# Kernel optimization log

Measured on AMD Instinct MI355X. Metric: run time of the kernel, lower is better.

The kernel has to match this reference:

```python
import jax, jax.numpy as jnp
import numpy as np

B, T, HID = 4, 2048, 1024
NH = 16
HS = HID // NH  # 64


def setup_inputs() -> dict:
    key = jax.random.key(0)
    ks = jax.random.split(key, 9)
    s = 1.0 / np.sqrt(HID)
    return {
        "x": jax.random.normal(ks[0], (B, T, HID), dtype=jnp.float32),
        "Wq": jax.random.uniform(ks[1], (HID, HID), jnp.float32, -s, s),
        "bq": jax.random.uniform(ks[2], (HID,), jnp.float32, -s, s),
        "Wk": jax.random.uniform(ks[3], (HID, HID), jnp.float32, -s, s),
        "bk": jax.random.uniform(ks[4], (HID,), jnp.float32, -s, s),
        "Wv": jax.random.uniform(ks[5], (HID, HS), jnp.float32, -s, s),
        "bv": jax.random.uniform(ks[6], (HS,), jnp.float32, -s, s),
        "Wo": jax.random.uniform(ks[7], (HS, HID), jnp.float32, -1.0 / np.sqrt(HS), 1.0 / np.sqrt(HS)),
        "bo": jax.random.uniform(ks[8], (HID,), jnp.float32, -1.0 / np.sqrt(HS), 1.0 / np.sqrt(HS)),
    }


def reference(x, Wq, bq, Wk, bk, Wv, bv, Wo, bo):
    scale = HS ** -0.5
    q = (x @ Wq + bq).reshape(B, T, NH, HS)  # (B,T,H,hs)
    k = (x @ Wk + bk).reshape(B, T, NH, HS)
    v = x @ Wv + bv                          # shared V: (B,T,hs)
    # scores: (B,H,T,T)
    scores = jnp.einsum("bqhd,bkhd->bhqk", q, k) * scale
    attn = jax.nn.softmax(scores, axis=-1)
    attn_avg = attn.mean(axis=1)             # (B,T,T), head-averaged
    out = jnp.einsum("bqk,bkd->bqd", attn_avg, v) @ Wo + bo  # (B,T,HID)
    return out, attn_avg
```

## Files before the change

kernel.cpp:

```cpp
#include <hip/hip_runtime.h>
#include <math.h>

#define Bc   4
#define Tt   2048
#define HIDc 1024
#define NHc  16
#define HSc  64
#define BTc  (Bc * Tt)
#define SCALE 0.125f

typedef __attribute__((ext_vector_type(8))) short bf16x8;
typedef __attribute__((ext_vector_type(4))) float f32x4;

__device__ __forceinline__ unsigned short f2bf(float f) {
    unsigned u = __float_as_uint(f);
    u = u + 0x7FFFu + ((u >> 16) & 1u);
    return (unsigned short)(u >> 16);
}

__global__ __launch_bounds__(256) void gemm_f32(
    const float* __restrict__ A, const float* __restrict__ Bm,
    const float* __restrict__ bias, float* __restrict__ C,
    int M, int N, int K, long sA, long sB, long sC)
{
    A  += (long)blockIdx.z * sA;
    Bm += (long)blockIdx.z * sB;
    C  += (long)blockIdx.z * sC;

    __shared__ float As[16][64];
    __shared__ float Bs[16][64];

    const int tid  = threadIdx.x;
    const int tx   = tid & 15;
    const int ty   = tid >> 4;
    const int row0 = blockIdx.y * 64;
    const int col0 = blockIdx.x * 64;

    const int la_r = tid >> 2;
    const int la_c = (tid & 3) << 2;
    const int lb_r = tid >> 4;
    const int lb_c = (tid & 15) << 2;

    float acc[4][4] = {};

    for (int k0 = 0; k0 < K; k0 += 16) {
        float4 av = *(const float4*)&A[(long)(row0 + la_r) * K + k0 + la_c];
        float4 bv = *(const float4*)&Bm[(long)(k0 + lb_r) * N + col0 + lb_c];
        __syncthreads();
        As[la_c + 0][la_r] = av.x;
        As[la_c + 1][la_r] = av.y;
        As[la_c + 2][la_r] = av.z;
        As[la_c + 3][la_r] = av.w;
        *(float4*)&Bs[lb_r][lb_c] = bv;
        __syncthreads();
#pragma unroll
        for (int kk = 0; kk < 16; ++kk) {
            float4 a = *(float4*)&As[kk][ty << 2];
            float4 b = *(float4*)&Bs[kk][tx << 2];
            float ar[4] = {a.x, a.y, a.z, a.w};
            float br[4] = {b.x, b.y, b.z, b.w};
#pragma unroll
            for (int i = 0; i < 4; ++i)
#pragma unroll
                for (int j = 0; j < 4; ++j)
                    acc[i][j] = fmaf(ar[i], br[j], acc[i][j]);
        }
    }

    float4 bvv = make_float4(0.f, 0.f, 0.f, 0.f);
    if (bias) bvv = *(const float4*)&bias[col0 + (tx << 2)];
#pragma unroll
    for (int i = 0; i < 4; ++i) {
        int m = row0 + (ty << 2) + i;
        float4 o;
        o.x = acc[i][0] + bvv.x;
        o.y = acc[i][1] + bvv.y;
        o.z = acc[i][2] + bvv.z;
        o.w = acc[i][3] + bvv.w;
        *(float4*)&C[(long)m * N + col0 + (tx << 2)] = o;
    }
}

__global__ __launch_bounds__(256) void gemm_skinny_splitk(
    const float* __restrict__ A, const float* __restrict__ Bm,
    float* __restrict__ C, int K, int KC, long sA, long sB, long sC)
{
    A  += (long)blockIdx.z * sA;
    Bm += (long)blockIdx.z * sB;
    C  += (long)blockIdx.z * sC;

    __shared__ float As[16][64];
    __shared__ float Bs[16][64];

    const int tid  = threadIdx.x;
    const int tx   = tid & 15;
    const int ty   = tid >> 4;
    const int row0 = blockIdx.x * 64;
    const int kbeg = blockIdx.y * KC;

    const int la_r = tid >> 2;
    const int la_c = (tid & 3) << 2;
    const int lb_r = tid >> 4;
    const int lb_c = (tid & 15) << 2;

    float acc[4][4] = {};

    for (int k0 = kbeg; k0 < kbeg + KC; k0 += 16) {
        float4 av = *(const float4*)&A[(long)(row0 + la_r) * K + k0 + la_c];
        float4 bv = *(const float4*)&Bm[(long)(k0 + lb_r) * 64 + lb_c];
        __syncthreads();
        As[la_c + 0][la_r] = av.x;
        As[la_c + 1][la_r] = av.y;
        As[la_c + 2][la_r] = av.z;
        As[la_c + 3][la_r] = av.w;
        *(float4*)&Bs[lb_r][lb_c] = bv;
        __syncthreads();
#pragma unroll
        for (int kk = 0; kk < 16; ++kk) {
            float4 a = *(float4*)&As[kk][ty << 2];
            float4 b = *(float4*)&Bs[kk][tx << 2];
            float ar[4] = {a.x, a.y, a.z, a.w};
            float br[4] = {b.x, b.y, b.z, b.w};
#pragma unroll
            for (int i = 0; i < 4; ++i)
#pragma unroll
                for (int j = 0; j < 4; ++j)
                    acc[i][j] = fmaf(ar[i], br[j], acc[i][j]);
        }
    }

#pragma unroll
    for (int i = 0; i < 4; ++i) {
        const int m = row0 + (ty << 2) + i;
#pragma unroll
        for (int j = 0; j < 4; ++j)
            atomicAdd(&C[(long)m * 64 + (tx << 2) + j], acc[i][j]);
    }
}

__global__ __launch_bounds__(256) void init_bias64(
    float* __restrict__ C, const float* __restrict__ bias, long n)
{
    long idx = (long)blockIdx.x * 256 + threadIdx.x;
    if (idx < n) C[idx] = bias ? bias[idx & 63] : 0.f;
}

__global__ __launch_bounds__(256) void cast_bf16(
    const float* __restrict__ src, unsigned short* __restrict__ dst, long n)
{
    long i = ((long)blockIdx.x * 256 + threadIdx.x) * 4;
    if (i >= n) return;
    float4 v = *(const float4*)&src[i];
    ushort4 o;
    o.x = f2bf(v.x); o.y = f2bf(v.y); o.z = f2bf(v.z); o.w = f2bf(v.w);
    *(ushort4*)&dst[i] = o;
}

__global__ __launch_bounds__(256) void transpose_cast(
    const float* __restrict__ W, unsigned short* __restrict__ Wt)
{
    __shared__ float t[32][33];
    const int k0 = blockIdx.x * 32, n0 = blockIdx.y * 32;
    const int c = threadIdx.x & 31, r = threadIdx.x >> 5;
#pragma unroll
    for (int rr = r; rr < 32; rr += 8)
        t[rr][c] = W[(long)(k0 + rr) * HIDc + n0 + c];
    __syncthreads();
#pragma unroll
    for (int rr = r; rr < 32; rr += 8)
        Wt[(long)(n0 + rr) * HIDc + k0 + c] = f2bf(t[c][rr]);
}

__global__ __launch_bounds__(256) void gemm_bt_bf16(
    const unsigned short* __restrict__ A, const unsigned short* __restrict__ Bt,
    const float* __restrict__ bias, unsigned short* __restrict__ C,
    int M, int N, int K)
{
    __shared__ unsigned short As[128][72];
    __shared__ unsigned short Bs[128][72];

    const int tid  = threadIdx.x;
    const int row0 = blockIdx.y * 128;
    const int col0 = blockIdx.x * 128;
    const int w  = tid >> 6, L = tid & 63;
    const int wm = (w & 1) * 64, wn = (w >> 1) * 64;
    const int lr = tid >> 3;
    const int lc = (tid & 7) * 8;
    const int ml = L & 15, q8 = (L >> 4) * 8, q4 = (L >> 4) * 4;

    f32x4 acc[4][4];
#pragma unroll
    for (int i = 0; i < 4; ++i)
#pragma unroll
        for (int j = 0; j < 4; ++j)
            acc[i][j] = (f32x4){0.f, 0.f, 0.f, 0.f};

    for (int k0 = 0; k0 < K; k0 += 64) {
        __syncthreads();
#pragma unroll
        for (int rr = 0; rr < 128; rr += 32) {
            *(float4*)&As[lr + rr][lc] = *(const float4*)&A[(long)(row0 + lr + rr) * K + k0 + lc];
            *(float4*)&Bs[lr + rr][lc] = *(const float4*)&Bt[(long)(col0 + lr + rr) * K + k0 + lc];
        }
        __syncthreads();
#pragma unroll
        for (int kk = 0; kk < 64; kk += 32) {
            bf16x8 a[4], b[4];
#pragma unroll
            for (int i = 0; i < 4; ++i) a[i] = *(bf16x8*)&As[wm + i * 16 + ml][kk + q8];
#pragma unroll
            for (int j = 0; j < 4; ++j) b[j] = *(bf16x8*)&Bs[wn + j * 16 + ml][kk + q8];
#pragma unroll
            for (int i = 0; i < 4; ++i)
#pragma unroll
                for (int j = 0; j < 4; ++j)
                    acc[i][j] = __builtin_amdgcn_mfma_f32_16x16x32_bf16(a[i], b[j], acc[i][j], 0, 0, 0);
        }
    }

#pragma unroll
    for (int j = 0; j < 4; ++j) {
        const int col = col0 + wn + j * 16 + ml;
        const float bj = bias ? bias[col] : 0.f;
#pragma unroll
        for (int i = 0; i < 4; ++i) {
#pragma unroll
            for (int r = 0; r < 4; ++r) {
                const int row = row0 + wm + i * 16 + q4 + r;
                C[(long)row * N + col] = f2bf(acc[i][j][r] + bj);
            }
        }
    }
}

__global__ __launch_bounds__(256) void attn_denom(
    const unsigned short* __restrict__ qb, const unsigned short* __restrict__ kb,
    float* __restrict__ linv)
{
    const int qt = blockIdx.x, h = blockIdx.y, b = blockIdx.z;
    __shared__ unsigned short Qs[64][72];
    __shared__ unsigned short Ks[64][72];
    __shared__ float lsum[64];

    const int tid = threadIdx.x;
    const int L = tid & 63, w = tid >> 6;
    const int rw = (w >> 1) * 32, kh = (w & 1) * 32;
    const int sr = tid >> 2, sc = (tid & 3) * 16;
    const int ml = L & 15, q8 = (L >> 4) * 8, q4 = (L >> 4) * 4;

    {
        const unsigned short* s = qb + ((long)(b * Tt + qt * 64 + sr) * HIDc + h * HSc + sc);
        *(float4*)&Qs[sr][sc]     = *(const float4*)s;
        *(float4*)&Qs[sr][sc + 8] = *(const float4*)(s + 8);
    }
    if (tid < 64) lsum[tid] = 0.f;

    float lacc[2][4] = {};

    for (int kt = 0; kt < Tt / 64; ++kt) {
        const unsigned short* s = kb + ((long)(b * Tt + kt * 64 + sr) * HIDc + h * HSc + sc);
        float4 v0 = *(const float4*)s;
        float4 v1 = *(const float4*)(s + 8);
        __syncthreads();
        *(float4*)&Ks[sr][sc]     = v0;
        *(float4*)&Ks[sr][sc + 8] = v1;
        __syncthreads();

        f32x4 acc[2][2];
#pragma unroll
        for (int i = 0; i < 2; ++i)
#pragma unroll
            for (int j = 0; j < 2; ++j) acc[i][j] = (f32x4){0.f, 0.f, 0.f, 0.f};
#pragma unroll
        for (int kk = 0; kk < 64; kk += 32) {
            bf16x8 a0 = *(bf16x8*)&Qs[rw + ml][kk + q8];
            bf16x8 a1 = *(bf16x8*)&Qs[rw + 16 + ml][kk + q8];
            bf16x8 b0 = *(bf16x8*)&Ks[kh + ml][kk + q8];
            bf16x8 b1 = *(bf16x8*)&Ks[kh + 16 + ml][kk + q8];
            acc[0][0] = __builtin_amdgcn_mfma_f32_16x16x32_bf16(a0, b0, acc[0][0], 0, 0, 0);
            acc[0][1] = __builtin_amdgcn_mfma_f32_16x16x32_bf16(a0, b1, acc[0][1], 0, 0, 0);
            acc[1][0] = __builtin_amdgcn_mfma_f32_16x16x32_bf16(a1, b0, acc[1][0], 0, 0, 0);
            acc[1][1] = __builtin_amdgcn_mfma_f32_16x16x32_bf16(a1, b1, acc[1][1], 0, 0, 0);
        }
#pragma unroll
        for (int i = 0; i < 2; ++i)
#pragma unroll
            for (int j = 0; j < 2; ++j)
#pragma unroll
                for (int r = 0; r < 4; ++r)
                    lacc[i][r] += __expf(acc[i][j][r] * SCALE);
    }

#pragma unroll
    for (int i = 0; i < 2; ++i)
#pragma unroll
        for (int r = 0; r < 4; ++r) {
            float v = lacc[i][r];
            v += __shfl_xor(v, 1, 16);
            v += __shfl_xor(v, 2, 16);
            v += __shfl_xor(v, 4, 16);
            v += __shfl_xor(v, 8, 16);
            if (ml == 0) atomicAdd(&lsum[rw + i * 16 + q4 + r], v);
        }
    __syncthreads();
    if (tid < 64)
        linv[((long)(b * NHc + h)) * Tt + qt * 64 + tid] = 1.0f / (lsum[tid] * (float)NHc);
}

__global__ __launch_bounds__(256) void attn_avg_w(
    const unsigned short* __restrict__ qb, const unsigned short* __restrict__ kb,
    const float* __restrict__ linv, const float* __restrict__ v,
    float* __restrict__ attn, float* __restrict__ o1)
{
    const int kt = blockIdx.x, qt = blockIdx.y, b = blockIdx.z;
    __shared__ unsigned short Qs[64][72];
    __shared__ unsigned short Ks[64][72];
    __shared__ unsigned short Ps[64][72];
    __shared__ unsigned short Vst[64][72];
    __shared__ float invs[64];

    const int tid = threadIdx.x;
    const int L = tid & 63, w = tid >> 6;
    const int rw = (w >> 1) * 32, kh = (w & 1) * 32;
    const int sr = tid >> 2, sc = (tid & 3) * 16;
    const int ml = L & 15, q8 = (L >> 4) * 8, q4 = (L >> 4) * 4;

#pragma unroll
    for (int e = tid; e < 4096; e += 256) {
        const int r = e >> 6, d = e & 63;
        Vst[d][r] = f2bf(v[((long)(b * Tt + kt * 64 + r)) * 64 + d]);
    }

    float pacc[2][2][4] = {};

    for (int h = 0; h < NHc; ++h) {
        const unsigned short* sq = qb + ((long)(b * Tt + qt * 64 + sr) * HIDc + h * HSc + sc);
        const unsigned short* sk = kb + ((long)(b * Tt + kt * 64 + sr) * HIDc + h * HSc + sc);
        float4 q0 = *(const float4*)sq;
        float4 q1 = *(const float4*)(sq + 8);
        float4 k0 = *(const float4*)sk;
        float4 k1 = *(const float4*)(sk + 8);
        float iv = 0.f;
        if (tid < 64) iv = linv[((long)(b * NHc + h)) * Tt + qt * 64 + tid];
        __syncthreads();
        *(float4*)&Qs[sr][sc]     = q0;
        *(float4*)&Qs[sr][sc + 8] = q1;
        *(float4*)&Ks[sr][sc]     = k0;
        *(float4*)&Ks[sr][sc + 8] = k1;
        if (tid < 64) invs[tid] = iv;
        __syncthreads();

        f32x4 acc[2][2];
#pragma unroll
        for (int i = 0; i < 2; ++i)
#pragma unroll
            for (int j = 0; j < 2; ++j) acc[i][j] = (f32x4){0.f, 0.f, 0.f, 0.f};
#pragma unroll
        for (int kk = 0; kk < 64; kk += 32) {
            bf16x8 a0 = *(bf16x8*)&Qs[rw + ml][kk + q8];
            bf16x8 a1 = *(bf16x8*)&Qs[rw + 16 + ml][kk + q8];
            bf16x8 b0 = *(bf16x8*)&Ks[kh + ml][kk + q8];
            bf16x8 b1 = *(bf16x8*)&Ks[kh + 16 + ml][kk + q8];
            acc[0][0] = __builtin_amdgcn_mfma_f32_16x16x32_bf16(a0, b0, acc[0][0], 0, 0, 0);
            acc[0][1] = __builtin_amdgcn_mfma_f32_16x16x32_bf16(a0, b1, acc[0][1], 0, 0, 0);
            acc[1][0] = __builtin_amdgcn_mfma_f32_16x16x32_bf16(a1, b0, acc[1][0], 0, 0, 0);
            acc[1][1] = __builtin_amdgcn_mfma_f32_16x16x32_bf16(a1, b1, acc[1][1], 0, 0, 0);
        }
#pragma unroll
        for (int i = 0; i < 2; ++i)
#pragma unroll
            for (int r = 0; r < 4; ++r) {
                const float iv_r = invs[rw + i * 16 + q4 + r];
#pragma unroll
                for (int j = 0; j < 2; ++j)
                    pacc[i][j][r] += __expf(acc[i][j][r] * SCALE) * iv_r;
            }
    }

#pragma unroll
    for (int i = 0; i < 2; ++i)
#pragma unroll
        for (int j = 0; j < 2; ++j)
#pragma unroll
            for (int r = 0; r < 4; ++r) {
                const int qrow = rw + i * 16 + q4 + r;
                const int kcol = kh + j * 16 + ml;
                attn[((long)(b * Tt + qt * 64 + qrow)) * Tt + kt * 64 + kcol] = pacc[i][j][r];
                Ps[qrow][kcol] = f2bf(pacc[i][j][r]);
            }
    __syncthreads();

    const int qh = rw, dh = kh;
    f32x4 uacc[2][2];
#pragma unroll
    for (int i = 0; i < 2; ++i)
#pragma unroll
        for (int j = 0; j < 2; ++j) uacc[i][j] = (f32x4){0.f, 0.f, 0.f, 0.f};
#pragma unroll
    for (int kk = 0; kk < 64; kk += 32) {
        bf16x8 a0 = *(bf16x8*)&Ps[qh + ml][kk + q8];
        bf16x8 a1 = *(bf16x8*)&Ps[qh + 16 + ml][kk + q8];
        bf16x8 b0 = *(bf16x8*)&Vst[dh + ml][kk + q8];
        bf16x8 b1 = *(bf16x8*)&Vst[dh + 16 + ml][kk + q8];
        uacc[0][0] = __builtin_amdgcn_mfma_f32_16x16x32_bf16(a0, b0, uacc[0][0], 0, 0, 0);
        uacc[0][1] = __builtin_amdgcn_mfma_f32_16x16x32_bf16(a0, b1, uacc[0][1], 0, 0, 0);
        uacc[1][0] = __builtin_amdgcn_mfma_f32_16x16x32_bf16(a1, b0, uacc[1][0], 0, 0, 0);
        uacc[1][1] = __builtin_amdgcn_mfma_f32_16x16x32_bf16(a1, b1, uacc[1][1], 0, 0, 0);
    }
#pragma unroll
    for (int i = 0; i < 2; ++i)
#pragma unroll
        for (int j = 0; j < 2; ++j)
#pragma unroll
            for (int r = 0; r < 4; ++r) {
                const long row = (long)(b * Tt + qt * 64 + qh + i * 16 + q4 + r);
                const int  d   = dh + j * 16 + ml;
                atomicAdd(&o1[row * 64 + d], uacc[i][j][r]);
            }
}

extern "C" void kernel_launch(void* const* d_in, const int* in_sizes, int n_in,
                              void* d_out, int out_size, void* d_ws, size_t ws_size,
                              hipStream_t stream)
{
    const float* x  = (const float*)d_in[0];
    const float* Wq = (const float*)d_in[1];
    const float* bq = (const float*)d_in[2];
    const float* Wk = (const float*)d_in[3];
    const float* bk = (const float*)d_in[4];
    const float* Wv = (const float*)d_in[5];
    const float* bv = (const float*)d_in[6];
    const float* Wo = (const float*)d_in[7];
    const float* bo = (const float*)d_in[8];

    float* out  = (float*)d_out;
    float* attn = out + (long)BTc * HIDc;

    unsigned short* xb  = (unsigned short*)d_ws;
    unsigned short* Wqt = xb  + (long)BTc * HIDc;
    unsigned short* Wkt = Wqt + (long)HIDc * HIDc;
    unsigned short* qb  = Wkt + (long)HIDc * HIDc;
    unsigned short* kb  = qb  + (long)BTc * HIDc;
    float* v    = (float*)(kb + (long)BTc * HIDc);
    float* linv = v    + (long)BTc * HSc;
    float* o1   = linv + (long)Bc * NHc * Tt;

    dim3 blk(256);

    cast_bf16<<<dim3((BTc * HIDc) / 1024), blk, 0, stream>>>(x, xb, (long)BTc * HIDc);
    transpose_cast<<<dim3(32, 32), blk, 0, stream>>>(Wq, Wqt);
    transpose_cast<<<dim3(32, 32), blk, 0, stream>>>(Wk, Wkt);
    init_bias64<<<dim3((BTc * HSc) / 256), blk, 0, stream>>>(v,  bv,      (long)BTc * HSc);
    init_bias64<<<dim3((BTc * HSc) / 256), blk, 0, stream>>>(o1, nullptr, (long)BTc * HSc);

    gemm_bt_bf16<<<dim3(HIDc / 128, BTc / 128), blk, 0, stream>>>(xb, Wqt, bq, qb, BTc, HIDc, HIDc);
    gemm_bt_bf16<<<dim3(HIDc / 128, BTc / 128), blk, 0, stream>>>(xb, Wkt, bk, kb, BTc, HIDc, HIDc);

    gemm_skinny_splitk<<<dim3(BTc / 64, HIDc / 128, 1), blk, 0, stream>>>(
        x, Wv, v, HIDc, 128, 0, 0, 0);

    attn_denom<<<dim3(Tt / 64, NHc, Bc), blk, 0, stream>>>(qb, kb, linv);

    attn_avg_w<<<dim3(Tt / 64, Tt / 64, Bc), blk, 0, stream>>>(qb, kb, linv, v, attn, o1);

    gemm_f32<<<dim3(HIDc / 64, BTc / 64, 1), blk, 0, stream>>>(o1, Wo, bo, out, BTc, HIDc, HSc, 0, 0, 0);
}
```

Before: 451.3 us.

## Fold softmax scale into Q, use exp2, enlarge attention tiles, MFMA V projection

Pre-scales Q by scale*log2(e) in the projection epilogue so the attention kernels can use the hardware exp2 instruction with no per-element multiply. Enlarges the attn_denom tile to 128 query rows and the attn_avg_w tile to 128 key columns, so each wave does more MFMAs per shared-memory load. The shared memory for Ps and Vst is overlaid on the Q/K buffers. The V projection moves from an fp32 split-K kernel to a bf16 MFMA kernel on the cast input, which adds precision loss in V and more register pressure from the larger tiles.

```diff
diff --git a/kernel.cpp b/kernel.cpp
--- a/kernel.cpp
+++ b/kernel.cpp
@@ -7,7 +7,7 @@
 #define NHc  16
 #define HSc  64
 #define BTc  (Bc * Tt)
-#define SCALE 0.125f
+#define QSCALE 0.18033688011112042f
 
 typedef __attribute__((ext_vector_type(8))) short bf16x8;
 typedef __attribute__((ext_vector_type(4))) float f32x4;
@@ -16,6 +16,14 @@
     unsigned u = __float_as_uint(f);
     u = u + 0x7FFFu + ((u >> 16) & 1u);
     return (unsigned short)(u >> 16);
+}
+
+__device__ __forceinline__ float fexp2(float x) {
+#if __has_builtin(__builtin_amdgcn_exp2f)
+    return __builtin_amdgcn_exp2f(x);
+#else
+    float r; asm("v_exp_f32 %0, %1" : "=v"(r) : "v"(x)); return r;
+#endif
 }
 
 __global__ __launch_bounds__(256) void gemm_f32(
@@ -81,63 +89,6 @@
     }
 }
 
-__global__ __launch_bounds__(256) void gemm_skinny_splitk(
-    const float* __restrict__ A, const float* __restrict__ Bm,
-    float* __restrict__ C, int K, int KC, long sA, long sB, long sC)
-{
-    A  += (long)blockIdx.z * sA;
-    Bm += (long)blockIdx.z * sB;
-    C  += (long)blockIdx.z * sC;
-
-    __shared__ float As[16][64];
-    __shared__ float Bs[16][64];
-
-    const int tid  = threadIdx.x;
-    const int tx   = tid & 15;
-    const int ty   = tid >> 4;
-    const int row0 = blockIdx.x * 64;
-    const int kbeg = blockIdx.y * KC;
-
-    const int la_r = tid >> 2;
-    const int la_c = (tid & 3) << 2;
-    const int lb_r = tid >> 4;
-    const int lb_c = (tid & 15) << 2;
-
-    float acc[4][4] = {};
-
-    for (int k0 = kbeg; k0 < kbeg + KC; k0 += 16) {
-        float4 av = *(const float4*)&A[(long)(row0 + la_r) * K + k0 + la_c];
-        float4 bv = *(const float4*)&Bm[(long)(k0 + lb_r) * 64 + lb_c];
-        __syncthreads();
-        As[la_c + 0][la_r] = av.x;
-        As[la_c + 1][la_r] = av.y;
-        As[la_c + 2][la_r] = av.z;
-        As[la_c + 3][la_r] = av.w;
-        *(float4*)&Bs[lb_r][lb_c] = bv;
-        __syncthreads();
-#pragma unroll
-        for (int kk = 0; kk < 16; ++kk) {
-            float4 a = *(float4*)&As[kk][ty << 2];
-            float4 b = *(float4*)&Bs[kk][tx << 2];
-            float ar[4] = {a.x, a.y, a.z, a.w};
-            float br[4] = {b.x, b.y, b.z, b.w};
-#pragma unroll
-            for (int i = 0; i < 4; ++i)
-#pragma unroll
-                for (int j = 0; j < 4; ++j)
-                    acc[i][j] = fmaf(ar[i], br[j], acc[i][j]);
-        }
-    }
-
-#pragma unroll
-    for (int i = 0; i < 4; ++i) {
-        const int m = row0 + (ty << 2) + i;
-#pragma unroll
-        for (int j = 0; j < 4; ++j)
-            atomicAdd(&C[(long)m * 64 + (tx << 2) + j], acc[i][j]);
-    }
-}
-
 __global__ __launch_bounds__(256) void init_bias64(
     float* __restrict__ C, const float* __restrict__ bias, long n)
 {
@@ -157,24 +108,24 @@
 }
 
 __global__ __launch_bounds__(256) void transpose_cast(
-    const float* __restrict__ W, unsigned short* __restrict__ Wt)
+    const float* __restrict__ W, unsigned short* __restrict__ Wt, int R, int C)
 {
     __shared__ float t[32][33];
     const int k0 = blockIdx.x * 32, n0 = blockIdx.y * 32;
     const int c = threadIdx.x & 31, r = threadIdx.x >> 5;
 #pragma unroll
     for (int rr = r; rr < 32; rr += 8)
-        t[rr][c] = W[(long)(k0 + rr) * HIDc + n0 + c];
+        t[rr][c] = W[(long)(k0 + rr) * C + n0 + c];
     __syncthreads();
 #pragma unroll
     for (int rr = r; rr < 32; rr += 8)
-        Wt[(long)(n0 + rr) * HIDc + k0 + c] = f2bf(t[c][rr]);
+        Wt[(long)(n0 + rr) * R + k0 + c] = f2bf(t[c][rr]);
 }
 
 __global__ __launch_bounds__(256) void gemm_bt_bf16(
     const unsigned short* __restrict__ A, const unsigned short* __restrict__ Bt,
     const float* __restrict__ bias, unsigned short* __restrict__ C,
-    int M, int N, int K)
+    int M, int N, int K, float oscale)
 {
     __shared__ unsigned short As[128][72];
     __shared__ unsigned short Bs[128][72];
@@ -227,10 +178,63 @@
 #pragma unroll
             for (int r = 0; r < 4; ++r) {
                 const int row = row0 + wm + i * 16 + q4 + r;
-                C[(long)row * N + col] = f2bf(acc[i][j][r] + bj);
+                C[(long)row * N + col] = f2bf((acc[i][j][r] + bj) * oscale);
             }
         }
     }
+}
+
+__global__ __launch_bounds__(256) void gemm_v_bf16(
+    const unsigned short* __restrict__ A, const unsigned short* __restrict__ Bt,
+    float* __restrict__ C)
+{
+    __shared__ unsigned short As[128][72];
+    __shared__ unsigned short Bs[64][72];
+
+    const int tid  = threadIdx.x;
+    const int row0 = blockIdx.x * 128;
+    const int kbeg = blockIdx.y * 256;
+    const int w = tid >> 6, L = tid & 63;
+    const int ml = L & 15, q8 = (L >> 4) * 8, q4 = (L >> 4) * 4;
+    const int ar = tid >> 3, ac = (tid & 7) * 8;
+    const int br = tid >> 2, bc = (tid & 3) * 16;
+
+    f32x4 acc[2][4];
+#pragma unroll
+    for (int i = 0; i < 2; ++i)
+#pragma unroll
+        for (int j = 0; j < 4; ++j) acc[i][j] = (f32x4){0.f, 0.f, 0.f, 0.f};
+
+    for (int k0 = kbeg; k0 < kbeg + 256; k0 += 64) {
+        __syncthreads();
+#pragma unroll
+        for (int rr = 0; rr < 128; rr += 32)
+            *(float4*)&As[ar + rr][ac] = *(const float4*)&A[(long)(row0 + ar + rr) * HIDc + k0 + ac];
+        *(float4*)&Bs[br][bc]     = *(const float4*)&Bt[(long)br * HIDc + k0 + bc];
+        *(float4*)&Bs[br][bc + 8] = *(const float4*)&Bt[(long)br * HIDc + k0 + bc + 8];
+        __syncthreads();
+#pragma unroll
+        for (int kk = 0; kk < 64; kk += 32) {
+            bf16x8 a[2], b[4];
+#pragma unroll
+            for (int i = 0; i < 2; ++i) a[i] = *(bf16x8*)&As[w * 32 + i * 16 + ml][kk + q8];
+#pragma unroll
+            for (int j = 0; j < 4; ++j) b[j] = *(bf16x8*)&Bs[j * 16 + ml][kk + q8];
+#pragma unroll
+            for (int i = 0; i < 2; ++i)
+#pragma unroll
+                for (int j = 0; j < 4; ++j)
+                    acc[i][j] = __builtin_amdgcn_mfma_f32_16x16x32_bf16(a[i], b[j], acc[i][j], 0, 0, 0);
+        }
+    }
+
+#pragma unroll
+    for (int i = 0; i < 2; ++i)
+#pragma unroll
+        for (int j = 0; j < 4; ++j)
+#pragma unroll
+            for (int r = 0; r < 4; ++r)
+                atomicAdd(&C[(long)(row0 + w * 32 + i * 16 + q4 + r) * 64 + j * 16 + ml], acc[i][j][r]);
 }
 
 __global__ __launch_bounds__(256) void attn_denom(
@@ -238,57 +242,56 @@
     float* __restrict__ linv)
 {
     const int qt = blockIdx.x, h = blockIdx.y, b = blockIdx.z;
-    __shared__ unsigned short Qs[64][72];
+    __shared__ unsigned short Qs[128][72];
     __shared__ unsigned short Ks[64][72];
-    __shared__ float lsum[64];
 
     const int tid = threadIdx.x;
-    const int L = tid & 63, w = tid >> 6;
-    const int rw = (w >> 1) * 32, kh = (w & 1) * 32;
-    const int sr = tid >> 2, sc = (tid & 3) * 16;
+    const int w = tid >> 6, L = tid & 63;
     const int ml = L & 15, q8 = (L >> 4) * 8, q4 = (L >> 4) * 4;
-
-    {
-        const unsigned short* s = qb + ((long)(b * Tt + qt * 64 + sr) * HIDc + h * HSc + sc);
-        *(float4*)&Qs[sr][sc]     = *(const float4*)s;
-        *(float4*)&Qs[sr][sc + 8] = *(const float4*)(s + 8);
-    }
-    if (tid < 64) lsum[tid] = 0.f;
+    const int ar = tid >> 3, ac = (tid & 7) * 8;
+    const int kr = tid >> 2, kc = (tid & 3) * 16;
+
+#pragma unroll
+    for (int rr = 0; rr < 128; rr += 32)
+        *(float4*)&Qs[ar + rr][ac] =
+            *(const float4*)&qb[(long)(b * Tt + qt * 128 + ar + rr) * HIDc + h * HSc + ac];
 
     float lacc[2][4] = {};
 
     for (int kt = 0; kt < Tt / 64; ++kt) {
-        const unsigned short* s = kb + ((long)(b * Tt + kt * 64 + sr) * HIDc + h * HSc + sc);
+        const unsigned short* s = kb + ((long)(b * Tt + kt * 64 + kr) * HIDc + h * HSc + kc);
         float4 v0 = *(const float4*)s;
         float4 v1 = *(const float4*)(s + 8);
         __syncthreads();
-        *(float4*)&Ks[sr][sc]     = v0;
-        *(float4*)&Ks[sr][sc + 8] = v1;
-        __syncthreads();
-
-        f32x4 acc[2][2];
+        *(float4*)&Ks[kr][kc]     = v0;
+        *(float4*)&Ks[kr][kc + 8] = v1;
+        __syncthreads();
+
+        f32x4 acc[2][4];
 #pragma unroll
         for (int i = 0; i < 2; ++i)
 #pragma unroll
-            for (int j = 0; j < 2; ++j) acc[i][j] = (f32x4){0.f, 0.f, 0.f, 0.f};
+            for (int j = 0; j < 4; ++j) acc[i][j] = (f32x4){0.f, 0.f, 0.f, 0.f};
 #pragma unroll
         for (int kk = 0; kk < 64; kk += 32) {
-            bf16x8 a0 = *(bf16x8*)&Qs[rw + ml][kk + q8];
-            bf16x8 a1 = *(bf16x8*)&Qs[rw + 16 + ml][kk + q8];
-            bf16x8 b0 = *(bf16x8*)&Ks[kh + ml][kk + q8];
-            bf16x8 b1 = *(bf16x8*)&Ks[kh + 16 + ml][kk + q8];
-            acc[0][0] = __builtin_amdgcn_mfma_f32_16x16x32_bf16(a0, b0, acc[0][0], 0, 0, 0);
-            acc[0][1] = __builtin_amdgcn_mfma_f32_16x16x32_bf16(a0, b1, acc[0][1], 0, 0, 0);
-            acc[1][0] = __builtin_amdgcn_mfma_f32_16x16x32_bf16(a1, b0, acc[1][0], 0, 0, 0);
-            acc[1][1] = __builtin_amdgcn_mfma_f32_16x16x32_bf16(a1, b1, acc[1][1], 0, 0, 0);
+            bf16x8 a[2], bfr[4];
+#pragma unroll
+            for (int i = 0; i < 2; ++i) a[i] = *(bf16x8*)&Qs[w * 32 + i * 16 + ml][kk + q8];
+#pragma unroll
+            for (int j = 0; j < 4; ++j) bfr[j] = *(bf16x8*)&Ks[j * 16 + ml][kk + q8];
+#pragma unroll
+            for (int i = 0; i < 2; ++i)
+#pragma unroll
+                for (int j = 0; j < 4; ++j)
+                    acc[i][j] = __builtin_amdgcn_mfma_f32_16x16x32_bf16(a[i], bfr[j], acc[i][j], 0, 0, 0);
         }
 #pragma unroll
         for (int i = 0; i < 2; ++i)
 #pragma unroll
-            for (int j = 0; j < 2; ++j)
+            for (int j = 0; j < 4; ++j)
 #pragma unroll
                 for (int r = 0; r < 4; ++r)
-                    lacc[i][r] += __expf(acc[i][j][r] * SCALE);
+                    lacc[i][r] += fexp2(acc[i][j][r]);
     }
 
 #pragma unroll
@@ -300,11 +303,10 @@
             v += __shfl_xor(v, 2, 16);
             v += __shfl_xor(v, 4, 16);
             v += __shfl_xor(v, 8, 16);
-            if (ml == 0) atomicAdd(&lsum[rw + i * 16 + q4 + r], v);
-        }
-    __syncthreads();
-    if (tid < 64)
-        linv[((long)(b * NHc + h)) * Tt + qt * 64 + tid] = 1.0f / (lsum[tid] * (float)NHc);
+            if (ml == 0)
+                linv[((long)(b * NHc + h)) * Tt + qt * 128 + w * 32 + i * 16 + q4 + r] =
+                    1.0f / (v * (float)NHc);
+        }
 }
 
 __global__ __launch_bounds__(256) void attn_avg_w(
@@ -312,92 +314,104 @@
     const float* __restrict__ linv, const float* __restrict__ v,
     float* __restrict__ attn, float* __restrict__ o1)
 {
-    const int kt = blockIdx.x, qt = blockIdx.y, b = blockIdx.z;
-    __shared__ unsigned short Qs[64][72];
-    __shared__ unsigned short Ks[64][72];
-    __shared__ unsigned short Ps[64][72];
-    __shared__ unsigned short Vst[64][72];
-    __shared__ float invs[64];
+    const int ktg = blockIdx.x, qt = blockIdx.y, b = blockIdx.z;
+
+    __shared__ __align__(16) unsigned char smem[34816];
+    unsigned short (*Qs)[72]   = (unsigned short(*)[72])smem;
+    unsigned short (*Ks)[72]   = (unsigned short(*)[72])(smem + 9216);
+    float* invs                = (float*)(smem + 27648);
+    unsigned short (*Ps)[136]  = (unsigned short(*)[136])smem;
+    unsigned short (*Vst)[136] = (unsigned short(*)[136])(smem + 17408);
 
     const int tid = threadIdx.x;
-    const int L = tid & 63, w = tid >> 6;
-    const int rw = (w >> 1) * 32, kh = (w & 1) * 32;
-    const int sr = tid >> 2, sc = (tid & 3) * 16;
+    const int w = tid >> 6, L = tid & 63;
     const int ml = L & 15, q8 = (L >> 4) * 8, q4 = (L >> 4) * 4;
-
-#pragma unroll
-    for (int e = tid; e < 4096; e += 256) {
-        const int r = e >> 6, d = e & 63;
-        Vst[d][r] = f2bf(v[((long)(b * Tt + kt * 64 + r)) * 64 + d]);
-    }
-
-    float pacc[2][2][4] = {};
+    const int rw = (w >> 1) * 32;
+    const int kh = (w & 1) * 64;
+    const int qr = tid >> 2, qc = (tid & 3) * 16;
+    const int kr = tid >> 3, kc = (tid & 7) * 8;
+
+    float pacc[2][4][4] = {};
 
     for (int h = 0; h < NHc; ++h) {
-        const unsigned short* sq = qb + ((long)(b * Tt + qt * 64 + sr) * HIDc + h * HSc + sc);
-        const unsigned short* sk = kb + ((long)(b * Tt + kt * 64 + sr) * HIDc + h * HSc + sc);
+        const unsigned short* sq = qb + ((long)(b * Tt + qt * 64 + qr) * HIDc + h * HSc + qc);
         float4 q0 = *(const float4*)sq;
         float4 q1 = *(const float4*)(sq + 8);
-        float4 k0 = *(const float4*)sk;
-        float4 k1 = *(const float4*)(sk + 8);
+        float4 kv[4];
+#pragma unroll
+        for (int rr = 0; rr < 4; ++rr)
+            kv[rr] = *(const float4*)&kb[(long)(b * Tt + ktg * 128 + kr + rr * 32) * HIDc + h * HSc + kc];
         float iv = 0.f;
         if (tid < 64) iv = linv[((long)(b * NHc + h)) * Tt + qt * 64 + tid];
         __syncthreads();
-        *(float4*)&Qs[sr][sc]     = q0;
-        *(float4*)&Qs[sr][sc + 8] = q1;
-        *(float4*)&Ks[sr][sc]     = k0;
-        *(float4*)&Ks[sr][sc + 8] = k1;
+        *(float4*)&Qs[qr][qc]     = q0;
+        *(float4*)&Qs[qr][qc + 8] = q1;
+#pragma unroll
+        for (int rr = 0; rr < 4; ++rr)
+            *(float4*)&Ks[kr + rr * 32][kc] = kv[rr];
         if (tid < 64) invs[tid] = iv;
         __syncthreads();
 
-        f32x4 acc[2][2];
+        f32x4 acc[2][4];
 #pragma unroll
         for (int i = 0; i < 2; ++i)
 #pragma unroll
-            for (int j = 0; j < 2; ++j) acc[i][j] = (f32x4){0.f, 0.f, 0.f, 0.f};
+            for (int j = 0; j < 4; ++j) acc[i][j] = (f32x4){0.f, 0.f, 0.f, 0.f};
 #pragma unroll
         for (int kk = 0; kk < 64; kk += 32) {
-            bf16x8 a0 = *(bf16x8*)&Qs[rw + ml][kk + q8];
-            bf16x8 a1 = *(bf16x8*)&Qs[rw + 16 + ml][kk + q8];
-            bf16x8 b0 = *(bf16x8*)&Ks[kh + ml][kk + q8];
-            bf16x8 b1 = *(bf16x8*)&Ks[kh + 16 + ml][kk + q8];
-            acc[0][0] = __builtin_amdgcn_mfma_f32_16x16x32_bf16(a0, b0, acc[0][0], 0, 0, 0);
-            acc[0][1] = __builtin_amdgcn_mfma_f32_16x16x32_bf16(a0, b1, acc[0][1], 0, 0, 0);
-            acc[1][0] = __builtin_amdgcn_mfma_f32_16x16x32_bf16(a1, b0, acc[1][0], 0, 0, 0);
-            acc[1][1] = __builtin_amdgcn_mfma_f32_16x16x32_bf16(a1, b1, acc[1][1], 0, 0, 0);
-        }
+            bf16x8 a[2], bfr[4];
+#pragma unroll
+            for (int i = 0; i < 2; ++i) a[i] = *(bf16x8*)&Qs[rw + i * 16 + ml][kk + q8];
+#pragma unroll
+            for (int j = 0; j < 4; ++j) bfr[j] = *(bf16x8*)&Ks[kh + j * 16 + ml][kk + q8];
+#pragma unroll
+            for (int i = 0; i < 2; ++i)
+#pragma unroll
+                for (int j = 0; j < 4; ++j)
+                    acc[i][j] = __builtin_amdgcn_mfma_f32_16x16x32_bf16(a[i], bfr[j], acc[i][j], 0, 0, 0);
+        }
+        float ivr[2][4];
 #pragma unroll
         for (int i = 0; i < 2; ++i)
 #pragma unroll
-            for (int r = 0; r < 4; ++r) {
-                const float iv_r = invs[rw + i * 16 + q4 + r];
-#pragma unroll
-                for (int j = 0; j < 2; ++j)
-                    pacc[i][j][r] += __expf(acc[i][j][r] * SCALE) * iv_r;
-            }
-    }
-
-#pragma unroll
-    for (int i = 0; i < 2; ++i)
-#pragma unroll
-        for (int j = 0; j < 2; ++j)
+            for (int r = 0; r < 4; ++r) ivr[i][r] = invs[rw + i * 16 + q4 + r];
+#pragma unroll
+        for (int i = 0; i < 2; ++i)
+#pragma unroll
+            for (int j = 0; j < 4; ++j)
+#pragma unroll
+                for (int r = 0; r < 4; ++r)
+                    pacc[i][j][r] += fexp2(acc[i][j][r]) * ivr[i][r];
+    }
+
+    __syncthreads();
+
+#pragma unroll
+    for (int i = 0; i < 2; ++i)
+#pragma unroll
+        for (int j = 0; j < 4; ++j)
 #pragma unroll
             for (int r = 0; r < 4; ++r) {
                 const int qrow = rw + i * 16 + q4 + r;
-                const int kcol = kh + j * 16 + ml;
-                attn[((long)(b * Tt + qt * 64 + qrow)) * Tt + kt * 64 + kcol] = pacc[i][j][r];
-                Ps[qrow][kcol] = f2bf(pacc[i][j][r]);
+                const int col  = kh + j * 16 + ml;
+                attn[((long)(b * Tt + qt * 64 + qrow)) * Tt + ktg * 128 + col] = pacc[i][j][r];
+                Ps[qrow][col] = f2bf(pacc[i][j][r]);
             }
+#pragma unroll
+    for (int e = tid; e < 8192; e += 256) {
+        const int r = e >> 6, d = e & 63;
+        Vst[d][r] = f2bf(v[((long)(b * Tt + ktg * 128 + r)) * 64 + d]);
+    }
     __syncthreads();
 
-    const int qh = rw, dh = kh;
+    const int qh = (w >> 1) * 32, dh = (w & 1) * 32;
     f32x4 uacc[2][2];
 #pragma unroll
     for (int i = 0; i < 2; ++i)
 #pragma unroll
         for (int j = 0; j < 2; ++j) uacc[i][j] = (f32x4){0.f, 0.f, 0.f, 0.f};
 #pragma unroll
-    for (int kk = 0; kk < 64; kk += 32) {
+    for (int kk = 0; kk < 128; kk += 32) {
         bf16x8 a0 = *(bf16x8*)&Ps[qh + ml][kk + q8];
         bf16x8 a1 = *(bf16x8*)&Ps[qh + 16 + ml][kk + q8];
         bf16x8 b0 = *(bf16x8*)&Vst[dh + ml][kk + q8];
@@ -412,11 +426,9 @@
 #pragma unroll
         for (int j = 0; j < 2; ++j)
 #pragma unroll
-            for (int r = 0; r < 4; ++r) {
-                const long row = (long)(b * Tt + qt * 64 + qh + i * 16 + q4 + r);
-                const int  d   = dh + j * 16 + ml;
-                atomicAdd(&o1[row * 64 + d], uacc[i][j][r]);
-            }
+            for (int r = 0; r < 4; ++r)
+                atomicAdd(&o1[((long)(b * Tt + qt * 64 + qh + i * 16 + q4 + r)) * 64 + dh + j * 16 + ml],
+                          uacc[i][j][r]);
 }
 
 extern "C" void kernel_launch(void* const* d_in, const int* in_sizes, int n_in,
@@ -439,7 +451,8 @@
     unsigned short* xb  = (unsigned short*)d_ws;
     unsigned short* Wqt = xb  + (long)BTc * HIDc;
     unsigned short* Wkt = Wqt + (long)HIDc * HIDc;
-    unsigned short* qb  = Wkt + (long)HIDc * HIDc;
+    unsigned short* Wvt = Wkt + (long)HIDc * HIDc;
+    unsigned short* qb  = Wvt + (long)HSc * HIDc;
     unsigned short* kb  = qb  + (long)BTc * HIDc;
     float* v    = (float*)(kb + (long)BTc * HIDc);
     float* linv = v    + (long)BTc * HSc;
@@ -448,20 +461,20 @@
     dim3 blk(256);
 
     cast_bf16<<<dim3((BTc * HIDc) / 1024), blk, 0, stream>>>(x, xb, (long)BTc * HIDc);
-    transpose_cast<<<dim3(32, 32), blk, 0, stream>>>(Wq, Wqt);
-    transpose_cast<<<dim3(32, 32), blk, 0, stream>>>(Wk, Wkt);
+    transpose_cast<<<dim3(32, 32), blk, 0, stream>>>(Wq, Wqt, HIDc, HIDc);
+    transpose_cast<<<dim3(32, 32), blk, 0, stream>>>(Wk, Wkt, HIDc, HIDc);
+    transpose_cast<<<dim3(32, 2),  blk, 0, stream>>>(Wv, Wvt, HIDc, HSc);
     init_bias64<<<dim3((BTc * HSc) / 256), blk, 0, stream>>>(v,  bv,      (long)BTc * HSc);
     init_bias64<<<dim3((BTc * HSc) / 256), blk, 0, stream>>>(o1, nullptr, (long)BTc * HSc);
 
-    gemm_bt_bf16<<<dim3(HIDc / 128, BTc / 128), blk, 0, stream>>>(xb, Wqt, bq, qb, BTc, HIDc, HIDc);
-    gemm_bt_bf16<<<dim3(HIDc / 128, BTc / 128), blk, 0, stream>>>(xb, Wkt, bk, kb, BTc, HIDc, HIDc);
-
-    gemm_skinny_splitk<<<dim3(BTc / 64, HIDc / 128, 1), blk, 0, stream>>>(
-        x, Wv, v, HIDc, 128, 0, 0, 0);
-
-    attn_denom<<<dim3(Tt / 64, NHc, Bc), blk, 0, stream>>>(qb, kb, linv);
-
-    attn_avg_w<<<dim3(Tt / 64, Tt / 64, Bc), blk, 0, stream>>>(qb, kb, linv, v, attn, o1);
+    gemm_bt_bf16<<<dim3(HIDc / 128, BTc / 128), blk, 0, stream>>>(xb, Wqt, bq, qb, BTc, HIDc, HIDc, QSCALE);
+    gemm_bt_bf16<<<dim3(HIDc / 128, BTc / 128), blk, 0, stream>>>(xb, Wkt, bk, kb, BTc, HIDc, HIDc, 1.0f);
+
+    gemm_v_bf16<<<dim3(BTc / 128, HIDc / 256), blk, 0, stream>>>(xb, Wvt, v);
+
+    attn_denom<<<dim3(Tt / 128, NHc, Bc), blk, 0, stream>>>(qb, kb, linv);
+
+    attn_avg_w<<<dim3(Tt / 128, Tt / 64, Bc), blk, 0, stream>>>(qb, kb, linv, v, attn, o1);
 
     gemm_f32<<<dim3(HIDc / 64, BTc / 64, 1), blk, 0, stream>>>(o1, Wo, bo, out, BTc, HIDc, HSc, 0, 0, 0);
 }
```

Result: no change. 449.0 us (-0.5%).
